# Kernel tuning notes

Measured on AMD Instinct MI355X. Metric: run time of the kernel, lower is better.

## Reference

```python
import jax, jax.numpy as jnp
import numpy as np
from jax import lax

B, L, D, DM, S, M, P = 8, 2048, 512, 1024, 32, 4, 4096


def setup_inputs() -> dict:
    key = jax.random.key(0)
    ks = jax.random.split(key, 13)
    emb = jax.random.normal(ks[0], (B, L, D), jnp.float32)
    pos = jax.random.randint(ks[1], (B, L), 1, P + 1)          # pos >= 1 (0 reserved for CLS)
    sid = jax.random.randint(ks[2], (B, L), 0, S)
    mod = jax.random.randint(ks[3], (B, L), 0, M)
    role = jax.random.randint(ks[4], (B, L), 0, 3)
    padding_mask = jax.random.uniform(ks[5], (B, L)) < 0.9
    W_proj = jax.random.normal(ks[6], (S, DM, D), jnp.float32) / np.float32(np.sqrt(D))
    b_proj = jax.random.normal(ks[7], (S, DM), jnp.float32) * 0.01
    cls_content = jax.random.normal(ks[8], (DM,), jnp.float32)
    pos_emb = jax.random.normal(ks[9], (P + 1, DM), jnp.float32) * 0.02
    id_emb = jax.random.normal(ks[10], (S + 1, DM), jnp.float32) * 0.02
    mod_emb = jax.random.normal(ks[11], (M, DM), jnp.float32) * 0.02
    role_emb = jax.random.normal(ks[12], (3, DM), jnp.float32) * 0.02
    return dict(emb=emb, pos=pos, sid=sid, mod=mod, role=role, padding_mask=padding_mask,
                W_proj=W_proj, b_proj=b_proj, cls_content=cls_content,
                pos_emb=pos_emb, id_emb=id_emb, mod_emb=mod_emb, role_emb=role_emb)


def _moe_project(emb, sid, padding_mask, W_proj, b_proj):
    """Per-token per-signal Linear: tokens[b,l] = W_proj[sid[b,l]] @ emb[b,l] + b_proj[sid[b,l]].
    Computed as S dense GEMMs masked per token (dense-dispatch MoE), avoiding an
    O(B*L*DM*D) gathered-weight tensor."""
    def step(acc, sWb):
        s, W, b = sWb
        y = jnp.einsum('bld,od->blo', emb, W) + b  # (B, L, DM)
        m = (sid == s) & padding_mask              # padded tokens stay zero
        return acc + jnp.where(m[..., None], y, 0.0), None
    acc0 = jnp.zeros(emb.shape[:2] + (W_proj.shape[1],), emb.dtype)
    acc, _ = lax.scan(step, acc0, (jnp.arange(W_proj.shape[0]), W_proj, b_proj))
    return acc


def reference(emb, pos, sid, mod, role, padding_mask,
              W_proj, b_proj, cls_content, pos_emb, id_emb, mod_emb, role_emb):
    Bc, Lc = pos.shape
    dm = cls_content.shape[0]
    cls_id = id_emb.shape[0] - 1  # == num_signals

    proj = _moe_project(emb, sid, padding_mask, W_proj, b_proj)  # (B, L, DM)

    cls = jnp.broadcast_to(cls_content, (Bc, 1, dm))
    tokens = jnp.concatenate([cls, proj], axis=1)                # (B, L+1, DM)

    pos_full = jnp.concatenate([jnp.zeros((Bc, 1), pos.dtype), pos], axis=1)
    sid_full = jnp.concatenate([jnp.full((Bc, 1), cls_id, sid.dtype), sid], axis=1)
    tokens = tokens + pos_emb[pos_full] + id_emb[sid_full]

    # modality + role embeddings only on non-CLS tokens (added even where padded, as in torch)
    tokens = tokens.at[:, 1:, :].add(mod_emb[mod] + role_emb[role])

    attn_keep = jnp.concatenate([jnp.ones((Bc, 1), bool), padding_mask], axis=1)
    return tokens, attn_keep
```

## Files before the change

### kernel.cpp

```cpp
#include <hip/hip_runtime.h>
#include <hip/hip_bf16.h>


#define NB   8
#define NL   2048
#define ND   512
#define NDM  1024
#define NS   32
#define NTOK (NB * NL)
#define LP1  (NL + 1)
#define MAXTILES 160
#define EXP_CAP 1024
#define EMB_ELEMS (NTOK * ND)
#define W_ELEMS (NS * NDM * ND)

static __device__ __forceinline__ size_t attn_off() { return (size_t)NB * LP1 * NDM; }

typedef __attribute__((ext_vector_type(8))) short bf16x8;
typedef __attribute__((ext_vector_type(4))) float f32x4;

__device__ __forceinline__ unsigned short f2bf(float f) {
    unsigned int x = __float_as_uint(f);
    x += 0x7fffu + ((x >> 16) & 1u);
    return (unsigned short)(x >> 16);
}

__device__ __forceinline__ bf16x8 cvt8(float4 a, float4 b) {
    bf16x8 r;
    r[0] = (short)f2bf(a.x); r[1] = (short)f2bf(a.y);
    r[2] = (short)f2bf(a.z); r[3] = (short)f2bf(a.w);
    r[4] = (short)f2bf(b.x); r[5] = (short)f2bf(b.y);
    r[6] = (short)f2bf(b.z); r[7] = (short)f2bf(b.w);
    return r;
}

__device__ __forceinline__ float4 ld4(const float* p) { return *(const float4*)p; }
__device__ __forceinline__ float4 add4(float4 a, float4 b) {
    return make_float4(a.x + b.x, a.y + b.y, a.z + b.z, a.w + b.w);
}

__global__ void k_bucket(const int* __restrict__ sid, const int* __restrict__ mask,
                         const int* __restrict__ pos, const int* __restrict__ mod,
                         const int* __restrict__ role,
                         int* __restrict__ cnt, int* __restrict__ restCnt,
                         int* __restrict__ tokList, int* __restrict__ restList,
                         float* __restrict__ out) {
    int t = blockIdx.x * 256 + threadIdx.x;
    if (t >= NTOK) return;
    int s = sid[t];
    bool keep = mask[t] != 0;
    int b = t >> 11, l = t & (NL - 1);
    out[attn_off() + (size_t)b * LP1 + l + 1] = keep ? 1.0f : 0.0f;
    if (t < NB) out[attn_off() + (size_t)t * LP1] = 1.0f;
    int mr = mod[t] * 3 + role[t];
    int packed = t | (pos[t] << 14) | (mr << 27);
    if (keep) {
        int idx = atomicAdd(&cnt[s], 1);
        if (idx < EXP_CAP) tokList[s * EXP_CAP + idx] = packed;
    } else {
        int ridx = atomicAdd(restCnt, 1);
        restList[ridx] = packed;
    }
}

__global__ void k_tiles(const int* __restrict__ cnt, int* __restrict__ meta,
                        int4* __restrict__ tiles,
                        const float* __restrict__ me, const float* __restrict__ re,
                        float* __restrict__ mrT) {
    if (threadIdx.x == 0) {
        int idx = 0;
        for (int e = 0; e < NS; ++e) {
            int c = min(cnt[e], EXP_CAP);
            for (int r = 0; r < c; r += 128)
                tiles[idx++] = make_int4(e, r, min(128, c - r), 0);
        }
        meta[0] = idx;
    }
    for (int i = threadIdx.x; i < 12 * (NDM / 4); i += 256) {
        int mr = i / (NDM / 4); int o = (i % (NDM / 4)) * 4;
        int m = mr / 3, ro = mr % 3;
        float4 v = add4(ld4(me + (size_t)m * NDM + o), ld4(re + (size_t)ro * NDM + o));
        *(float4*)&mrT[(size_t)mr * NDM + o] = v;
    }
}

__global__ void k_cvt(const float* __restrict__ emb, const float* __restrict__ W,
                      short* __restrict__ embBf, short* __restrict__ wBf) {
    size_t i = ((size_t)blockIdx.x * 256 + threadIdx.x) * 16;
    const float* src; short* dst;
    if (i < (size_t)EMB_ELEMS) { src = emb + i; dst = embBf + i; }
    else { src = W + (i - EMB_ELEMS); dst = wBf + (i - EMB_ELEMS); }
    float4 a = ld4(src), b = ld4(src + 4), c = ld4(src + 8), d = ld4(src + 12);
    *(bf16x8*)dst       = cvt8(a, b);
    *(bf16x8*)(dst + 8) = cvt8(c, d);
}

__global__ __launch_bounds__(256, 3) void k_gemm(
    const short* __restrict__ embBf, const short* __restrict__ wBf,
    const int* __restrict__ tokList, const int4* __restrict__ tiles,
    const int* __restrict__ meta,
    const float* __restrict__ bp, const float* __restrict__ pe,
    const float* __restrict__ ie, const float* __restrict__ mrT,
    float* __restrict__ out) {
    if (blockIdx.x >= meta[0]) return;
    int4 td = tiles[blockIdx.x];
    const int e = td.x, rowBase = td.y, nRows = td.z;
    const int nBase = blockIdx.y * 128;

    __shared__ short SA[128 * 32];
    __shared__ short SB[128 * 32];

    const int tid  = threadIdx.x;
    const int lane = tid & 63;
    const int w    = tid >> 6;
    const int wr   = w >> 1, wc = w & 1;
    const int fr   = lane & 15, kg = lane >> 4;

    const int srow = tid >> 2;
    const int sch  = tid & 3;
    const size_t eBase = (size_t)e * EXP_CAP + rowBase;
    int ar0 = (srow < nRows) ? srow : 0;
    int ar1 = (srow + 64 < nRows) ? srow + 64 : 0;
    int tok0 = tokList[eBase + ar0] & 16383;
    int tok1 = tokList[eBase + ar1] & 16383;
    const short* a0 = embBf + (size_t)tok0 * ND + sch * 8;
    const short* a1 = embBf + (size_t)tok1 * ND + sch * 8;
    const short* b0 = wBf + ((size_t)e * NDM + nBase + srow) * ND + sch * 8;
    const short* b1 = wBf + ((size_t)e * NDM + nBase + srow + 64) * ND + sch * 8;
    const int wo0 = srow * 32 + (sch ^ ((srow >> 1) & 3)) * 8;
    const int wo1 = wo0 + 64 * 32;

    const float* bpE = bp + (size_t)e * NDM;
    const float* ieE = ie + (size_t)e * NDM;
    float eb[4]; int colv[4];
#pragma unroll
    for (int j = 0; j < 4; ++j) {
        colv[j] = nBase + wc * 64 + j * 16 + fr;
        eb[j] = bpE[colv[j]] + ieE[colv[j]];
    }

    f32x4 acc[4][4];
#pragma unroll
    for (int i = 0; i < 4; ++i)
#pragma unroll
        for (int j = 0; j < 4; ++j)
            acc[i][j] = (f32x4){0.f, 0.f, 0.f, 0.f};

    bf16x8 ra0 = *(const bf16x8*)a0;
    bf16x8 ra1 = *(const bf16x8*)a1;
    bf16x8 rb0 = *(const bf16x8*)b0;
    bf16x8 rb1 = *(const bf16x8*)b1;

    const int pc = kg ^ ((fr >> 1) & 3);
    for (int ks = 0; ks < ND / 32; ++ks) {
        __syncthreads();
        *(bf16x8*)&SA[wo0] = ra0;
        *(bf16x8*)&SA[wo1] = ra1;
        *(bf16x8*)&SB[wo0] = rb0;
        *(bf16x8*)&SB[wo1] = rb1;
        __syncthreads();
        if (ks < ND / 32 - 1) {
            ra0 = *(const bf16x8*)(a0 + (ks + 1) * 32);
            ra1 = *(const bf16x8*)(a1 + (ks + 1) * 32);
            rb0 = *(const bf16x8*)(b0 + (ks + 1) * 32);
            rb1 = *(const bf16x8*)(b1 + (ks + 1) * 32);
        }
        bf16x8 af[4], bv[4];
#pragma unroll
        for (int i = 0; i < 4; ++i)
            af[i] = *(const bf16x8*)&SA[(wr * 64 + i * 16 + fr) * 32 + pc * 8];
#pragma unroll
        for (int j = 0; j < 4; ++j)
            bv[j] = *(const bf16x8*)&SB[(wc * 64 + j * 16 + fr) * 32 + pc * 8];
#pragma unroll
        for (int i = 0; i < 4; ++i)
#pragma unroll
            for (int j = 0; j < 4; ++j)
                acc[i][j] = __builtin_amdgcn_mfma_f32_16x16x32_bf16(af[i], bv[j], acc[i][j], 0, 0, 0);
    }

#pragma unroll
    for (int i = 0; i < 4; ++i) {
#pragma unroll
        for (int r = 0; r < 4; ++r) {
            int row = wr * 64 + i * 16 + kg * 4 + r;
            if (row < nRows) {
                int pk = tokList[eBase + row];
                int t = pk & 16383, p = (pk >> 14) & 8191, mr = (pk >> 27) & 15;
                const float* peR = pe + (size_t)p * NDM;
                const float* mrR = mrT + (size_t)mr * NDM;
                size_t orow = ((size_t)(t >> 11) * LP1 + (t & (NL - 1)) + 1) * NDM;
#pragma unroll
                for (int j = 0; j < 4; ++j)
                    out[orow + colv[j]] = acc[i][j][r] + eb[j] + peR[colv[j]] + mrR[colv[j]];
            }
        }
    }
}

__global__ void k_rest(const int* __restrict__ sid,
                       const int* __restrict__ restList, const int* __restrict__ meta,
                       const float* __restrict__ cls_c, const float* __restrict__ pos_e,
                       const float* __restrict__ id_e, const float* __restrict__ mrT,
                       float* __restrict__ out) {
    int total = meta[1] + NB;
    int half = threadIdx.x >> 7;
    int o = (threadIdx.x & 127) * 8;
    for (int rI = blockIdx.x * 2 + half; rI < total; rI += gridDim.x * 2) {
        float4 v0, v1; size_t orow;
        if (rI < NB) {
            const float* ieC = id_e + (size_t)NS * NDM;
            v0 = add4(add4(ld4(cls_c + o), ld4(pos_e + o)), ld4(ieC + o));
            v1 = add4(add4(ld4(cls_c + o + 4), ld4(pos_e + o + 4)), ld4(ieC + o + 4));
            orow = (size_t)rI * LP1 * NDM;
        } else {
            int pk = restList[rI - NB];
            int t = pk & 16383, p = (pk >> 14) & 8191, mr = (pk >> 27) & 15;
            int s = sid[t];
            const float* peR = pos_e + (size_t)p * NDM;
            const float* ieR = id_e + (size_t)s * NDM;
            const float* mrR = mrT + (size_t)mr * NDM;
            v0 = add4(add4(ld4(peR + o), ld4(ieR + o)), ld4(mrR + o));
            v1 = add4(add4(ld4(peR + o + 4), ld4(ieR + o + 4)), ld4(mrR + o + 4));
            orow = ((size_t)(t >> 11) * LP1 + (t & (NL - 1)) + 1) * NDM;
        }
        *(float4*)&out[orow + o] = v0;
        *(float4*)&out[orow + o + 4] = v1;
    }
}

extern "C" void kernel_launch(void* const* d_in, const int* in_sizes, int n_in,
                              void* d_out, int out_size, void* d_ws, size_t ws_size,
                              hipStream_t stream) {
    const float* emb  = (const float*)d_in[0];
    const int* pos    = (const int*)d_in[1];
    const int* sid    = (const int*)d_in[2];
    const int* mod    = (const int*)d_in[3];
    const int* role   = (const int*)d_in[4];
    const int* mask   = (const int*)d_in[5];
    const float* Wp   = (const float*)d_in[6];
    const float* bp   = (const float*)d_in[7];
    const float* cls  = (const float*)d_in[8];
    const float* pe   = (const float*)d_in[9];
    const float* ie   = (const float*)d_in[10];
    const float* me   = (const float*)d_in[11];
    const float* re   = (const float*)d_in[12];
    float* out = (float*)d_out;

    int* ws        = (int*)d_ws;
    int* cnt       = ws;
    int* meta      = ws + 32;
    int4* tiles    = (int4*)(ws + 128);
    int* tokList   = ws + 1024;
    int* restList  = ws + 33792;
    float* mrT     = (float*)(ws + 50176);
    short* embBf   = (short*)((char*)d_ws + 262144);
    short* wBf     = (short*)((char*)d_ws + 262144 + (size_t)EMB_ELEMS * 2);

    hipMemsetAsync(ws, 0, 64 * sizeof(int), stream);
    k_bucket<<<NTOK / 256, 256, 0, stream>>>(sid, mask, pos, mod, role,
                                             cnt, meta + 1, tokList, restList, out);
    k_tiles<<<1, 256, 0, stream>>>(cnt, meta, tiles, me, re, mrT);
    k_cvt<<<(EMB_ELEMS + W_ELEMS) / (256 * 16), 256, 0, stream>>>(emb, Wp, embBf, wBf);

    dim3 gg(MAXTILES, NDM / 128);
    k_gemm<<<gg, 256, 0, stream>>>(embBf, wBf, tokList, tiles, meta,
                                   bp, pe, ie, mrT, out);
    k_rest<<<512, 256, 0, stream>>>(sid, restList, meta, cls, pe, ie, mrT, out);
}
```

Before: 134.5 us.

## Write GEMM results to compact bf16 buffer and add embeddings in coalesced pass

The GEMM epilogue no longer scatters fp32 rows with gathered positional and mode embedding reads. It now writes bf16 results into a compact per-expert buffer. A new dense output kernel walks every (batch, position) row in order and adds the embeddings, bias and compact projection with coalesced float4 stores, replacing the separate rest kernel. This trades an extra bf16 write/read round trip, plus a second rounding of the projection to bf16, for coalesced output writes and a lighter GEMM epilogue. The GEMM launch bounds also go from 3 to 4 blocks per CU.

```diff
diff --git a/kernel.cpp b/kernel.cpp
--- a/kernel.cpp
+++ b/kernel.cpp
@@ -25,6 +25,10 @@
     return (unsigned short)(x >> 16);
 }
 
+__device__ __forceinline__ float bf2f(unsigned short s) {
+    return __uint_as_float(((unsigned int)s) << 16);
+}
+
 __device__ __forceinline__ bf16x8 cvt8(float4 a, float4 b) {
     bf16x8 r;
     r[0] = (short)f2bf(a.x); r[1] = (short)f2bf(a.y);
@@ -40,11 +44,8 @@
 }
 
 __global__ void k_bucket(const int* __restrict__ sid, const int* __restrict__ mask,
-                         const int* __restrict__ pos, const int* __restrict__ mod,
-                         const int* __restrict__ role,
-                         int* __restrict__ cnt, int* __restrict__ restCnt,
-                         int* __restrict__ tokList, int* __restrict__ restList,
-                         float* __restrict__ out) {
+                         int* __restrict__ cnt, int* __restrict__ kidx,
+                         int* __restrict__ tokList, float* __restrict__ out) {
     int t = blockIdx.x * 256 + threadIdx.x;
     if (t >= NTOK) return;
     int s = sid[t];
@@ -52,27 +53,26 @@
     int b = t >> 11, l = t & (NL - 1);
     out[attn_off() + (size_t)b * LP1 + l + 1] = keep ? 1.0f : 0.0f;
     if (t < NB) out[attn_off() + (size_t)t * LP1] = 1.0f;
-    int mr = mod[t] * 3 + role[t];
-    int packed = t | (pos[t] << 14) | (mr << 27);
+    int ki = -1;
     if (keep) {
-        int idx = atomicAdd(&cnt[s], 1);
-        if (idx < EXP_CAP) tokList[s * EXP_CAP + idx] = packed;
-    } else {
-        int ridx = atomicAdd(restCnt, 1);
-        restList[ridx] = packed;
-    }
+        ki = atomicAdd(&cnt[s], 1);
+        if (ki < EXP_CAP) tokList[s * EXP_CAP + ki] = t;
+    }
+    kidx[t] = ki;
 }
 
 __global__ void k_tiles(const int* __restrict__ cnt, int* __restrict__ meta,
-                        int4* __restrict__ tiles,
+                        int* __restrict__ bOff, int4* __restrict__ tiles,
                         const float* __restrict__ me, const float* __restrict__ re,
                         float* __restrict__ mrT) {
     if (threadIdx.x == 0) {
-        int idx = 0;
+        int idx = 0, cbase = 0;
         for (int e = 0; e < NS; ++e) {
             int c = min(cnt[e], EXP_CAP);
+            bOff[e] = cbase;
             for (int r = 0; r < c; r += 128)
-                tiles[idx++] = make_int4(e, r, min(128, c - r), 0);
+                tiles[idx++] = make_int4(e, r, min(128, c - r), cbase + r);
+            cbase += c;
         }
         meta[0] = idx;
     }
@@ -95,16 +95,13 @@
     *(bf16x8*)(dst + 8) = cvt8(c, d);
 }
 
-__global__ __launch_bounds__(256, 3) void k_gemm(
+__global__ __launch_bounds__(256, 4) void k_gemm(
     const short* __restrict__ embBf, const short* __restrict__ wBf,
     const int* __restrict__ tokList, const int4* __restrict__ tiles,
-    const int* __restrict__ meta,
-    const float* __restrict__ bp, const float* __restrict__ pe,
-    const float* __restrict__ ie, const float* __restrict__ mrT,
-    float* __restrict__ out) {
+    const int* __restrict__ meta, unsigned short* __restrict__ projC) {
     if (blockIdx.x >= meta[0]) return;
     int4 td = tiles[blockIdx.x];
-    const int e = td.x, rowBase = td.y, nRows = td.z;
+    const int e = td.x, rowBase = td.y, nRows = td.z, cBase = td.w;
     const int nBase = blockIdx.y * 128;
 
     __shared__ short SA[128 * 32];
@@ -121,23 +118,14 @@
     const size_t eBase = (size_t)e * EXP_CAP + rowBase;
     int ar0 = (srow < nRows) ? srow : 0;
     int ar1 = (srow + 64 < nRows) ? srow + 64 : 0;
-    int tok0 = tokList[eBase + ar0] & 16383;
-    int tok1 = tokList[eBase + ar1] & 16383;
+    int tok0 = tokList[eBase + ar0];
+    int tok1 = tokList[eBase + ar1];
     const short* a0 = embBf + (size_t)tok0 * ND + sch * 8;
     const short* a1 = embBf + (size_t)tok1 * ND + sch * 8;
     const short* b0 = wBf + ((size_t)e * NDM + nBase + srow) * ND + sch * 8;
     const short* b1 = wBf + ((size_t)e * NDM + nBase + srow + 64) * ND + sch * 8;
     const int wo0 = srow * 32 + (sch ^ ((srow >> 1) & 3)) * 8;
     const int wo1 = wo0 + 64 * 32;
-
-    const float* bpE = bp + (size_t)e * NDM;
-    const float* ieE = ie + (size_t)e * NDM;
-    float eb[4]; int colv[4];
-#pragma unroll
-    for (int j = 0; j < 4; ++j) {
-        colv[j] = nBase + wc * 64 + j * 16 + fr;
-        eb[j] = bpE[colv[j]] + ieE[colv[j]];
-    }
 
     f32x4 acc[4][4];
 #pragma unroll
@@ -185,48 +173,46 @@
         for (int r = 0; r < 4; ++r) {
             int row = wr * 64 + i * 16 + kg * 4 + r;
             if (row < nRows) {
-                int pk = tokList[eBase + row];
-                int t = pk & 16383, p = (pk >> 14) & 8191, mr = (pk >> 27) & 15;
-                const float* peR = pe + (size_t)p * NDM;
-                const float* mrR = mrT + (size_t)mr * NDM;
-                size_t orow = ((size_t)(t >> 11) * LP1 + (t & (NL - 1)) + 1) * NDM;
+                size_t crow = (size_t)(cBase + row) * NDM + nBase;
 #pragma unroll
                 for (int j = 0; j < 4; ++j)
-                    out[orow + colv[j]] = acc[i][j][r] + eb[j] + peR[colv[j]] + mrR[colv[j]];
+                    projC[crow + wc * 64 + j * 16 + fr] = f2bf(acc[i][j][r]);
             }
         }
     }
 }
 
-__global__ void k_rest(const int* __restrict__ sid,
-                       const int* __restrict__ restList, const int* __restrict__ meta,
-                       const float* __restrict__ cls_c, const float* __restrict__ pos_e,
-                       const float* __restrict__ id_e, const float* __restrict__ mrT,
-                       float* __restrict__ out) {
-    int total = meta[1] + NB;
-    int half = threadIdx.x >> 7;
-    int o = (threadIdx.x & 127) * 8;
-    for (int rI = blockIdx.x * 2 + half; rI < total; rI += gridDim.x * 2) {
-        float4 v0, v1; size_t orow;
-        if (rI < NB) {
-            const float* ieC = id_e + (size_t)NS * NDM;
-            v0 = add4(add4(ld4(cls_c + o), ld4(pos_e + o)), ld4(ieC + o));
-            v1 = add4(add4(ld4(cls_c + o + 4), ld4(pos_e + o + 4)), ld4(ieC + o + 4));
-            orow = (size_t)rI * LP1 * NDM;
-        } else {
-            int pk = restList[rI - NB];
-            int t = pk & 16383, p = (pk >> 14) & 8191, mr = (pk >> 27) & 15;
-            int s = sid[t];
-            const float* peR = pos_e + (size_t)p * NDM;
-            const float* ieR = id_e + (size_t)s * NDM;
-            const float* mrR = mrT + (size_t)mr * NDM;
-            v0 = add4(add4(ld4(peR + o), ld4(ieR + o)), ld4(mrR + o));
-            v1 = add4(add4(ld4(peR + o + 4), ld4(ieR + o + 4)), ld4(mrR + o + 4));
-            orow = ((size_t)(t >> 11) * LP1 + (t & (NL - 1)) + 1) * NDM;
-        }
-        *(float4*)&out[orow + o] = v0;
-        *(float4*)&out[orow + o + 4] = v1;
-    }
+__global__ void k_out(const int* __restrict__ pos, const int* __restrict__ sid,
+                      const int* __restrict__ mod, const int* __restrict__ role,
+                      const int* __restrict__ mask, const int* __restrict__ kidx,
+                      const int* __restrict__ bOff,
+                      const float* __restrict__ bp, const float* __restrict__ cls_c,
+                      const float* __restrict__ pe, const float* __restrict__ ie,
+                      const float* __restrict__ mrT,
+                      const unsigned short* __restrict__ projC,
+                      float* __restrict__ out) {
+    int l1 = blockIdx.x;
+    int b  = blockIdx.y;
+    int o  = threadIdx.x * 4;
+    float4 v;
+    if (l1 == 0) {
+        v = add4(add4(ld4(cls_c + o), ld4(pe + o)), ld4(ie + (size_t)NS * NDM + o));
+    } else {
+        int t = b * NL + l1 - 1;
+        int p = pos[t], s = sid[t], mr = mod[t] * 3 + role[t];
+        v = add4(ld4(pe + (size_t)p * NDM + o), ld4(ie + (size_t)s * NDM + o));
+        v = add4(v, ld4(mrT + (size_t)mr * NDM + o));
+        if (mask[t] != 0) {
+            v = add4(v, ld4(bp + (size_t)s * NDM + o));
+            int ki = kidx[t];
+            if (ki >= 0 && ki < EXP_CAP) {
+                const unsigned short* pr = projC + (size_t)(bOff[s] + ki) * NDM + o;
+                v.x += bf2f(pr[0]); v.y += bf2f(pr[1]);
+                v.z += bf2f(pr[2]); v.w += bf2f(pr[3]);
+            }
+        }
+    }
+    *(float4*)&out[((size_t)b * LP1 + l1) * NDM + o] = v;
 }
 
 extern "C" void kernel_launch(void* const* d_in, const int* in_sizes, int n_in,
@@ -250,21 +236,25 @@
     int* ws        = (int*)d_ws;
     int* cnt       = ws;
     int* meta      = ws + 32;
+    int* bOff      = ws + 64;
     int4* tiles    = (int4*)(ws + 128);
     int* tokList   = ws + 1024;
-    int* restList  = ws + 33792;
+    int* kidx      = ws + 33792;
     float* mrT     = (float*)(ws + 50176);
     short* embBf   = (short*)((char*)d_ws + 262144);
     short* wBf     = (short*)((char*)d_ws + 262144 + (size_t)EMB_ELEMS * 2);
+    unsigned short* projC = (unsigned short*)((char*)d_ws + 262144 +
+                              (size_t)EMB_ELEMS * 2 + (size_t)W_ELEMS * 2);
 
     hipMemsetAsync(ws, 0, 64 * sizeof(int), stream);
-    k_bucket<<<NTOK / 256, 256, 0, stream>>>(sid, mask, pos, mod, role,
-                                             cnt, meta + 1, tokList, restList, out);
-    k_tiles<<<1, 256, 0, stream>>>(cnt, meta, tiles, me, re, mrT);
+    k_bucket<<<NTOK / 256, 256, 0, stream>>>(sid, mask, cnt, kidx, tokList, out);
+    k_tiles<<<1, 256, 0, stream>>>(cnt, meta, bOff, tiles, me, re, mrT);
     k_cvt<<<(EMB_ELEMS + W_ELEMS) / (256 * 16), 256, 0, stream>>>(emb, Wp, embBf, wBf);
 
     dim3 gg(MAXTILES, NDM / 128);
-    k_gemm<<<gg, 256, 0, stream>>>(embBf, wBf, tokList, tiles, meta,
-                                   bp, pe, ie, mrT, out);
-    k_rest<<<512, 256, 0, stream>>>(sid, restList, meta, cls, pe, ie, mrT, out);
-}
+    k_gemm<<<gg, 256, 0, stream>>>(embBf, wBf, tokList, tiles, meta, projC);
+
+    dim3 go(LP1, NB);
+    k_out<<<go, 256, 0, stream>>>(pos, sid, mod, role, mask, kidx, bOff,
+                                  bp, cls, pe, ie, mrT, projC, out);
+}
```

After: 136.0 us. About the same (+1.1%).
